# Performance work log

Measured on AMD Instinct MI355X. Metric: run time of the kernel, lower is better.

## Reference

```python
import jax, jax.numpy as jnp
import numpy as np

B, C, S = 256, 1024, 14   # batch, channels, spatial (frozen by y.view(b,c,14,14))
C2 = 15                   # channels2 in the module
CAT = C // 2 * 3 + C2     # 1551 = 15 + 512 + 1024
EPS = 1e-5


def _conv(x, w, b, groups, pad):
    out = jax.lax.conv_general_dilated(
        x, w, window_strides=(1, 1), padding=((pad, pad), (pad, pad)),
        dimension_numbers=('NCHW', 'OIHW', 'NCHW'), feature_group_count=groups)
    return out + b[None, :, None, None]


def _bn(x, gamma, beta):
    # training-mode BatchNorm2d: biased batch stats over (N,H,W)
    m = x.mean((0, 2, 3), keepdims=True)
    v = x.var((0, 2, 3), keepdims=True)
    return (x - m) * jax.lax.rsqrt(v + EPS) * gamma[None, :, None, None] + beta[None, :, None, None]


def setup_inputs() -> dict:
    key = jax.random.key(0)
    ks = jax.random.split(key, 16)
    r = C2 // 7  # = 2
    inp = {
        'y': jax.random.normal(ks[0], (B, C2, S * S), jnp.float32),
        'x': jax.random.normal(ks[1], (B, C, S, S), jnp.float32),
        'fc1_w': jax.random.normal(ks[2], (r, C2), jnp.float32) * 0.2,
        'fc2_w': jax.random.normal(ks[3], (C2, r), jnp.float32) * 0.2,
        'conv_w': jax.random.normal(ks[4], (C // 2, C, 1, 1), jnp.float32) * 0.03,
        'conv_b': jnp.zeros((C // 2,), jnp.float32),
        'dconv_w': jax.random.normal(ks[5], (C, 1, 3, 3), jnp.float32) * 0.2,
        'dconv_b': jnp.zeros((C,), jnp.float32),
        'dw1_w': jax.random.normal(ks[6], (CAT, 1, 3, 3), jnp.float32) * 0.2,
        'dw1_b': jnp.zeros((CAT,), jnp.float32),
        'pw1_w': jax.random.normal(ks[7], (C // 2, CAT, 1, 1), jnp.float32) * 0.03,
        'pw1_b': jnp.zeros((C // 2,), jnp.float32),
        'gamma': jnp.ones((C // 2,), jnp.float32),
        'beta': jnp.zeros((C // 2,), jnp.float32),
        'n': 0,
    }
    return inp


def reference(y, x, fc1_w, fc2_w, conv_w, conv_b, dconv_w, dconv_b,
              dw1_w, dw1_b, pw1_w, pw1_b, gamma, beta, n):
    b = y.shape[0]
    y4 = y.reshape(b, C2, S, S)
    # SE block on the 15 sub-channels
    g = y4.mean((2, 3))                              # (b, 15) global avg pool
    h = jax.nn.relu(g @ fc1_w.T) @ fc2_w.T           # (b, 15)
    y1 = y4 * jax.nn.sigmoid(h)[:, :, None, None]
    # depthwise conv on x, then per-(b,c) row covariance of the 14x14 map
    x1 = _conv(x, dconv_w, dconv_b, C, 1)            # (b, C, 14, 14)
    x2 = jax.lax.stop_gradient(x1)                   # .detach() in the original
    xc = x2 - x2.mean(-1, keepdims=True)             # np.cov: rows=vars, cols=obs
    cov = jnp.einsum('bcik,bcjk->bcij', xc, xc) / (S - 1)
    z = _conv(cov, conv_w, conv_b, 1, 0)             # 1x1 conv C -> C//2
    z = jax.nn.sigmoid(_bn(z, gamma, beta))
    for _ in range(n):                               # n=0 at these shapes
        y1 = jax.image.resize(y1, (y1.shape[0], y1.shape[1], y1.shape[2] * 2, y1.shape[3] * 2), 'bilinear')
    cat = jnp.concatenate([y1, z, x], axis=1)        # (b, 1551, 14, 14)
    o = _conv(cat, dw1_w, dw1_b, CAT, 1)             # depthwise 3x3
    o = _conv(o, pw1_w, pw1_b, 1, 0)                 # pointwise 1x1 -> C//2
    return jax.nn.relu(_bn(o, gamma, beta))
```

## Files before the change

kernel.cpp:

```cpp
#include <hip/hip_runtime.h>

typedef unsigned int u32;
typedef unsigned short u16;
typedef __attribute__((ext_vector_type(8))) short bf16x8;
typedef __attribute__((ext_vector_type(4))) float f32x4;
typedef __attribute__((ext_vector_type(4))) u32 u32x4;

#define EPSBN 1e-5f

#define GLDS16(gp, lp) __builtin_amdgcn_global_load_lds( \
    (const __attribute__((address_space(1))) u32*)(gp), \
    (__attribute__((address_space(3))) u32*)(lp), 16, 0, 0)

#define OFF_ADW    0ull
#define OFF_COVT   0ull
#define OFF_S      160563200ull
#define OFF_WBZ    160578560ull
#define OFF_WBP    161627136ull
#define OFF_STATSZ 163265536ull
#define OFF_STATSO 163269632ull
#define OFF_SCZ    163273728ull
#define OFF_SHZ    163275776ull
#define OFF_SCO    163277824ull
#define OFF_SHO    163279872ull

static __device__ __forceinline__ float bf2f(u16 h){
  u32 u = ((u32)h) << 16; float f; __builtin_memcpy(&f, &u, 4); return f;
}
static __device__ __forceinline__ u16 f2bf(float f){
  u32 u; __builtin_memcpy(&u, &f, 4);
  u = (u + 0x7fffu + ((u >> 16) & 1u)) >> 16;
  return (u16)u;
}

__global__ __launch_bounds__(64) void se_kernel(const float* __restrict__ y,
    const float* __restrict__ fc1, const float* __restrict__ fc2, float* __restrict__ sse){
  __shared__ float g[15];
  __shared__ float t[2];
  int b = blockIdx.x, l = threadIdx.x;
  for (int c = 0; c < 15; ++c){
    float p = 0.f;
    for (int k = l; k < 196; k += 64) p += y[((size_t)b*15 + c)*196 + k];
    p += __shfl_xor(p, 32); p += __shfl_xor(p, 16); p += __shfl_xor(p, 8);
    p += __shfl_xor(p, 4);  p += __shfl_xor(p, 2);  p += __shfl_xor(p, 1);
    if (l == 0) g[c] = p * (1.f/196.f);
  }
  __syncthreads();
  if (l < 2){
    float a = 0.f;
    for (int c = 0; c < 15; ++c) a += g[c] * fc1[l*15 + c];
    t[l] = fmaxf(a, 0.f);
  }
  __syncthreads();
  if (l < 15){
    float h = t[0]*fc2[l*2] + t[1]*fc2[l*2+1];
    sse[b*15 + l] = 1.f / (1.f + __expf(-h));
  }
}

__global__ void wconv_kernel(const float* __restrict__ cw, const float* __restrict__ pw,
                             u16* __restrict__ wbz, u16* __restrict__ wbp){
  u32 stride = gridDim.x * blockDim.x;
  for (u32 i = blockIdx.x*blockDim.x + threadIdx.x; i < 524288u; i += stride)
    wbz[i] = f2bf(cw[i]);
  for (u32 i = blockIdx.x*blockDim.x + threadIdx.x; i < 819200u; i += stride){
    u32 n = i / 1600u, k = i - n*1600u;
    wbp[i] = f2bf(k < 1551u ? pw[(size_t)n*1551 + k] : 0.f);
  }
}

__global__ __launch_bounds__(256,5) void cov_kernel(const float* __restrict__ x,
    const float* __restrict__ dcw, const float* __restrict__ dcb, u16* __restrict__ covT){
  __shared__ __align__(16) float xs[16*200];
  __shared__ __align__(16) u32 xcb[16*132];
  __shared__ float wls[16][9];
  __shared__ float wlb[16];
  u32* covL32 = (u32*)xs;

  int tid = threadIdx.x;
  int c0 = blockIdx.x * 16, b = blockIdx.y;

  {
    const float4* xg = (const float4*)(x + ((size_t)b*1024 + c0)*196);
    for (int i = tid; i < 784; i += 256){
      float4 v = xg[i];
      u32 c = (u32)i / 49u, p4 = (u32)i - c*49u;
      *(float4*)&xs[c*200u + p4*4u] = v;
    }
  }
  if (tid < 144) wls[tid/9][tid%9] = dcw[(size_t)(c0 + tid/9)*9 + (tid%9)];
  if (tid < 16) wlb[tid] = dcb[c0 + tid];
  __syncthreads();

  {
    int c = tid >> 4, i = tid & 15;
    u32 q[8];
    #pragma unroll
    for (int j = 0; j < 8; ++j) q[j] = 0u;
    if (i < 14){
      float wr[9];
      #pragma unroll
      for (int qq = 0; qq < 9; ++qq) wr[qq] = wls[c][qq];
      float topm = (i > 0) ? 1.f : 0.f, botm = (i < 13) ? 1.f : 0.f;
      wr[0] *= topm; wr[1] *= topm; wr[2] *= topm;
      wr[6] *= botm; wr[7] *= botm; wr[8] *= botm;
      float bb = wlb[c];
      float rr[3][16];
      #pragma unroll
      for (int d = 0; d < 3; ++d){
        rr[d][0] = 0.f; rr[d][15] = 0.f;
        int rowr = i + d - 1;
        rowr = rowr < 0 ? 0 : (rowr > 13 ? 13 : rowr);
        const float* src = &xs[c*200 + rowr*14];
        #pragma unroll
        for (int j = 0; j < 7; ++j)
          *(float2*)&rr[d][1 + 2*j] = *(const float2*)&src[2*j];
      }
      float ov[14];
      #pragma unroll
      for (int k = 0; k < 14; ++k){
        float a = bb;
        #pragma unroll
        for (int dy = 0; dy < 3; ++dy)
          #pragma unroll
          for (int dx = 0; dx < 3; ++dx)
            a += wr[dy*3+dx] * rr[dy][k + dx];
        ov[k] = a;
      }
      float mean = 0.f;
      #pragma unroll
      for (int k = 0; k < 14; ++k) mean += ov[k];
      mean *= (1.f/14.f);
      #pragma unroll
      for (int j = 0; j < 7; ++j){
        u32 lo = f2bf(ov[2*j]   - mean);
        u32 hi = f2bf(ov[2*j+1] - mean);
        q[j] = lo | (hi << 16);
      }
    }
    u32x4 q0 = {q[0], q[1], q[2], q[3]};
    u32x4 q1 = {q[4], q[5], q[6], q[7]};
    *(u32x4*)&xcb[c*132 + i*8]     = q0;
    *(u32x4*)&xcb[c*132 + i*8 + 4] = q1;
  }
  __syncthreads();

  {
    int w = tid >> 6, l = tid & 63, lr = l & 15, lq = l >> 4;
    #pragma unroll
    for (int pp = 0; pp < 2; ++pp){
      int clo = w*4 + 2*pp;
      bf16x8 alo = {0,0,0,0,0,0,0,0}, ahi = {0,0,0,0,0,0,0,0};
      if (lq < 2){
        alo = *(const bf16x8*)&xcb[clo*132 + lr*8 + lq*4];
        ahi = *(const bf16x8*)&xcb[(clo+1)*132 + lr*8 + lq*4];
      }
      f32x4 dlo = {0.f,0.f,0.f,0.f}, dhi = {0.f,0.f,0.f,0.f};
      dlo = __builtin_amdgcn_mfma_f32_16x16x32_bf16(alo, alo, dlo, 0, 0, 0);
      dhi = __builtin_amdgcn_mfma_f32_16x16x32_bf16(ahi, ahi, dhi, 0, 0, 0);
      if (lr < 14){
        int cp = w*2 + pp;
        #pragma unroll
        for (int r = 0; r < 4; ++r){
          int rowi = lq*4 + r;
          if (rowi < 14){
            u32 vv = (u32)f2bf(dlo[r] * (1.f/13.f)) | ((u32)f2bf(dhi[r] * (1.f/13.f)) << 16);
            covL32[cp*210 + rowi*14 + lr] = vv;
          }
        }
      }
    }
  }
  __syncthreads();

  for (int i = tid; i < 1568; i += 256){
    int cp = i & 7, ij = i >> 3;
    u32 v = covL32[cp*210 + ij];
    *(u32*)(covT + ((size_t)(b*196 + ij)*1024 + c0 + 2*cp)) = v;
  }
}

__global__ __launch_bounds__(256,5) void adw_kernel(
    const float* __restrict__ y, const float* __restrict__ sse,
    const u16* __restrict__ zT, const float* __restrict__ scz, const float* __restrict__ shz,
    const float* __restrict__ x, const float* __restrict__ dw1w, const float* __restrict__ dw1b,
    u16* __restrict__ Adw){
  __shared__ __align__(16) float ms[32*202];
  __shared__ float wd[32][9];
  __shared__ float bd[32];
  int tid = threadIdx.x;
  int cc0 = blockIdx.x * 32, b = blockIdx.y;

  for (int i = tid; i < 288; i += 256){
    int c = i / 9, q = i - c*9;
    int cc = cc0 + c;
    wd[c][q] = (cc < 1551) ? dw1w[(size_t)cc*9 + q] : 0.f;
  }
  if (tid < 32) bd[tid] = (cc0 + tid < 1551) ? dw1b[cc0 + tid] : 0.f;

  if (cc0 < 15){
    int ny = 15;
    for (int i = tid; i < ny*196; i += 256){
      u32 c = (u32)i / 196u, p = (u32)i - c*196u;
      ms[c*202u + p] = y[((size_t)b*15 + c)*196 + p] * sse[b*15 + c];
    }
  }
  {
    int zs = cc0 > 15 ? cc0 : 15;
    int ze = cc0 + 32 < 527 ? cc0 + 32 : 527;
    if (zs < ze){
      int nz = ze - zs, lbase = zs - cc0, obase = zs - 15;
      const u16* zrow = zT + (size_t)obase*50176 + (size_t)b*196;
      for (int i = tid; i < nz*98; i += 256){
        u32 oo = (u32)i / 98u, pp = (u32)i - oo*98u;
        u32 v = *(const u32*)(zrow + (size_t)oo*50176 + pp*2u);
        int o = obase + (int)oo;
        float s = scz[o], h = shz[o];
        float v0 = bf2f((u16)(v & 0xffffu)) * s + h;
        float v1 = bf2f((u16)(v >> 16))     * s + h;
        v0 = 1.f / (1.f + __expf(-v0));
        v1 = 1.f / (1.f + __expf(-v1));
        float2 fv = {v0, v1};
        *(float2*)&ms[(u32)(lbase + (int)oo)*202u + pp*2u] = fv;
      }
    }
  }
  {
    int xs_ = cc0 > 527 ? cc0 : 527;
    int xe = cc0 + 32 < 1551 ? cc0 + 32 : 1551;
    if (xs_ < xe){
      int nx = xe - xs_, lbase = xs_ - cc0, cxs = xs_ - 527;
      const float4* xg = (const float4*)(x + ((size_t)b*1024 + cxs)*196);
      for (int i = tid; i < nx*49; i += 256){
        float4 v = xg[i];
        u32 c = (u32)i / 49u, p4 = (u32)i - c*49u;
        float* dst = &ms[(u32)(lbase + (int)c)*202u + p4*4u];
        float2 lo = {v.x, v.y}, hi = {v.z, v.w};
        *(float2*)dst = lo;
        *(float2*)(dst + 2) = hi;
      }
    }
  }
  {
    int ps = cc0 > 1551 ? cc0 : 1551;
    int pe = cc0 + 32;
    if (ps < pe){
      int np = pe - ps, lbase = ps - cc0;
      for (int i = tid; i < np*196; i += 256){
        u32 c = (u32)i / 196u, p = (u32)i - c*196u;
        ms[(u32)(lbase + (int)c)*202u + p] = 0.f;
      }
    }
  }
  __syncthreads();

  for (int t = tid; t < 448; t += 256){
    int cc = t & 31, i = t >> 5;
    float wr[9];
    #pragma unroll
    for (int qq = 0; qq < 9; ++qq) wr[qq] = wd[cc][qq];
    float topm = (i > 0) ? 1.f : 0.f, botm = (i < 13) ? 1.f : 0.f;
    wr[0] *= topm; wr[1] *= topm; wr[2] *= topm;
    wr[6] *= botm; wr[7] *= botm; wr[8] *= botm;
    float bb = bd[cc];
    float rr[3][16];
    #pragma unroll
    for (int d = 0; d < 3; ++d){
      rr[d][0] = 0.f; rr[d][15] = 0.f;
      int rowr = i + d - 1;
      rowr = rowr < 0 ? 0 : (rowr > 13 ? 13 : rowr);
      const float* src = &ms[cc*202 + rowr*14];
      #pragma unroll
      for (int j = 0; j < 7; ++j)
        *(float2*)&rr[d][1 + 2*j] = *(const float2*)&src[2*j];
    }
    size_t obase = ((size_t)b*196 + i*14) * 1600 + cc0 + cc;
    #pragma unroll
    for (int k = 0; k < 14; ++k){
      float a = bb;
      #pragma unroll
      for (int dy = 0; dy < 3; ++dy)
        #pragma unroll
        for (int dx = 0; dx < 3; ++dx)
          a += wr[dy*3+dx] * rr[dy][k + dx];
      Adw[obase + (size_t)k*1600] = f2bf(a);
    }
  }
}

template<int MODE>
__global__ __launch_bounds__(256,3) void gemm_kernel(
    const u16* __restrict__ A, const u16* __restrict__ Bw,
    const float* __restrict__ bias, void* __restrict__ outp,
    float* __restrict__ stats, int K){
  __shared__ __align__(16) char smem[33280];
  u16* As = (u16*)smem;
  u16* Bs = (u16*)(smem + 16384);

  int tid = threadIdx.x;
  int w = tid >> 6, l = tid & 63;
  int wm = w >> 1, wn = w & 1;
  int lr = l & 15, lq = l >> 4;
  u32 g = blockIdx.x;
  u32 lin = (g & 7u) * 196u + (g >> 3);
  int n0 = (int)(lin & 3u) * 128;
  int m0 = (int)(lin >> 2) * 128;

  f32x4 acc[4][4] = {};
  int kTiles = K >> 6;

  for (int kt = 0; kt < kTiles; ++kt){
    if (kt) __syncthreads();
    #pragma unroll
    for (int i = 0; i < 4; ++i){
      int s = tid + i*256;
      int row = s >> 3, c8 = s & 7, sc = c8 ^ (row & 7);
      GLDS16(A  + (size_t)(m0 + row)*K + kt*64 + sc*8, As + s*8);
      GLDS16(Bw + (size_t)(n0 + row)*K + kt*64 + sc*8, Bs + s*8);
    }
    __syncthreads();
    #pragma unroll
    for (int ks = 0; ks < 2; ++ks){
      bf16x8 af[4], bfv[4];
      #pragma unroll
      for (int mi = 0; mi < 4; ++mi){
        int row = wm*64 + mi*16 + lr;
        int q = (ks*4 + lq) ^ (row & 7);
        af[mi] = *(const bf16x8*)(As + row*64 + q*8);
      }
      #pragma unroll
      for (int ni = 0; ni < 4; ++ni){
        int row = wn*64 + ni*16 + lr;
        int q = (ks*4 + lq) ^ (row & 7);
        bfv[ni] = *(const bf16x8*)(Bs + row*64 + q*8);
      }
      #pragma unroll
      for (int mi = 0; mi < 4; ++mi)
        #pragma unroll
        for (int ni = 0; ni < 4; ++ni)
          acc[mi][ni] = __builtin_amdgcn_mfma_f32_16x16x32_bf16(af[mi], bfv[ni], acc[mi][ni], 0, 0, 0);
    }
  }

  #pragma unroll
  for (int ni = 0; ni < 4; ++ni){
    int col = n0 + wn*64 + ni*16 + lr;
    float bb = bias[col];
    float s1 = 0.f, s2 = 0.f;
    #pragma unroll
    for (int mi = 0; mi < 4; ++mi)
      #pragma unroll
      for (int r = 0; r < 4; ++r){
        float v = acc[mi][ni][r] + bb;
        acc[mi][ni][r] = v;
        s1 += v; s2 += v*v;
      }
    s1 += __shfl_xor(s1, 16); s1 += __shfl_xor(s1, 32);
    s2 += __shfl_xor(s2, 16); s2 += __shfl_xor(s2, 32);
    if (lq == 0){
      atomicAdd(&stats[col], s1);
      atomicAdd(&stats[512 + col], s2);
    }
  }

  __syncthreads();
  float* eb = (float*)smem;
  #pragma unroll
  for (int rnd = 0; rnd < 2; ++rnd){
    if (wm == rnd){
      float* e = eb + wn * (64*65);
      #pragma unroll
      for (int mi = 0; mi < 4; ++mi)
        #pragma unroll
        for (int ni = 0; ni < 4; ++ni)
          #pragma unroll
          for (int r = 0; r < 4; ++r)
            e[(mi*16 + lq*4 + r)*65 + ni*16 + lr] = acc[mi][ni][r];
      int m = m0 + wm*64 + l;
      if (MODE == 0){
        u16* ob = (u16*)outp + (size_t)(n0 + wn*64)*50176 + m;
        #pragma unroll 8
        for (int no = 0; no < 64; ++no)
          ob[(size_t)no*50176] = f2bf(e[l*65 + no]);
      } else {
        u32 bq = (u32)m / 196u;
        u32 ij = (u32)m - bq*196u;
        float* ob = (float*)outp + ((size_t)bq*512 + n0 + wn*64)*196 + ij;
        #pragma unroll 8
        for (int no = 0; no < 64; ++no)
          ob[(size_t)no*196] = e[l*65 + no];
      }
    }
    __syncthreads();
  }
}

__global__ void bnprep_kernel(const float* __restrict__ stats, const float* __restrict__ gamma,
    const float* __restrict__ beta, float* __restrict__ sc, float* __restrict__ sh){
  int o = threadIdx.x;
  float m = stats[o] * (1.f/50176.f);
  float v = stats[512+o] * (1.f/50176.f) - m*m;
  float inv = rsqrtf(v + EPSBN);
  float g = gamma[o] * inv;
  sc[o] = g;
  sh[o] = beta[o] - m*g;
}

__global__ void final_kernel(float4* __restrict__ o4, const float* __restrict__ sc,
                             const float* __restrict__ sh){
  u32 stride = gridDim.x * blockDim.x;
  for (u32 i = blockIdx.x*blockDim.x + threadIdx.x; i < 6422528u; i += stride){
    u32 oc = (i / 49u) & 511u;
    float s = sc[oc], t = sh[oc];
    float4 v = o4[i];
    v.x = fmaxf(fmaf(v.x, s, t), 0.f);
    v.y = fmaxf(fmaf(v.y, s, t), 0.f);
    v.z = fmaxf(fmaf(v.z, s, t), 0.f);
    v.w = fmaxf(fmaf(v.w, s, t), 0.f);
    o4[i] = v;
  }
}

extern "C" void kernel_launch(void* const* d_in, const int* in_sizes, int n_in,
                              void* d_out, int out_size, void* d_ws, size_t ws_size,
                              hipStream_t stream){
  (void)in_sizes; (void)n_in; (void)out_size; (void)ws_size;
  const float* y      = (const float*)d_in[0];
  const float* x      = (const float*)d_in[1];
  const float* fc1    = (const float*)d_in[2];
  const float* fc2    = (const float*)d_in[3];
  const float* convw  = (const float*)d_in[4];
  const float* convb  = (const float*)d_in[5];
  const float* dconvw = (const float*)d_in[6];
  const float* dconvb = (const float*)d_in[7];
  const float* dw1w   = (const float*)d_in[8];
  const float* dw1b   = (const float*)d_in[9];
  const float* pw1w   = (const float*)d_in[10];
  const float* pw1b   = (const float*)d_in[11];
  const float* gamma  = (const float*)d_in[12];
  const float* beta   = (const float*)d_in[13];

  char* ws = (char*)d_ws;
  u16* covT   = (u16*)(ws + OFF_COVT);
  u16* Adw    = (u16*)(ws + OFF_ADW);
  float* sse  = (float*)(ws + OFF_S);
  u16* wbz    = (u16*)(ws + OFF_WBZ);
  u16* wbp    = (u16*)(ws + OFF_WBP);
  float* statsZ = (float*)(ws + OFF_STATSZ);
  float* statsO = (float*)(ws + OFF_STATSO);
  float* scz  = (float*)(ws + OFF_SCZ);
  float* shz  = (float*)(ws + OFF_SHZ);
  float* sco  = (float*)(ws + OFF_SCO);
  float* sho  = (float*)(ws + OFF_SHO);
  u16* zT     = (u16*)d_out;
  float* outf = (float*)d_out;

  hipMemsetAsync(statsZ, 0, 8192, stream);
  se_kernel<<<256, 64, 0, stream>>>(y, fc1, fc2, sse);
  wconv_kernel<<<2048, 256, 0, stream>>>(convw, pw1w, wbz, wbp);
  cov_kernel<<<dim3(64, 256), 256, 0, stream>>>(x, dconvw, dconvb, covT);
  gemm_kernel<0><<<1568, 256, 0, stream>>>(covT, wbz, convb, (void*)zT, statsZ, 1024);
  bnprep_kernel<<<1, 512, 0, stream>>>(statsZ, gamma, beta, scz, shz);
  adw_kernel<<<dim3(50, 256), 256, 0, stream>>>(y, sse, zT, scz, shz, x, dw1w, dw1b, Adw);
  gemm_kernel<1><<<1568, 256, 0, stream>>>(Adw, wbp, pw1b, (void*)outf, statsO, 1600);
  bnprep_kernel<<<1, 512, 0, stream>>>(statsO, gamma, beta, sco, sho);
  final_kernel<<<8192, 256, 0, stream>>>((float4*)outf, sco, sho);
}
```

Before: 516.6 us.

## Double-buffer GEMM LDS tiles to overlap global loads with MFMA compute

The GEMM K-loop now keeps two LDS buffers and prefetches the next 64-wide K tile with global_load_lds while MFMAs run on the current tile. This removes the load-then-compute serialization and one barrier per iteration. In exchange, LDS per block doubles to 64 KB and launch bounds drop from 3 to 2 blocks per CU, which lowers occupancy. The epilogue now reuses the same LDS array and relies on the loop's trailing barrier.

Result: no change. 526.8 us (+2.0%).

```diff
diff --git a/kernel.cpp b/kernel.cpp
--- a/kernel.cpp
+++ b/kernel.cpp
@@ -289,13 +289,11 @@
 }
 
 template<int MODE>
-__global__ __launch_bounds__(256,3) void gemm_kernel(
+__global__ __launch_bounds__(256,2) void gemm_kernel(
     const u16* __restrict__ A, const u16* __restrict__ Bw,
     const float* __restrict__ bias, void* __restrict__ outp,
     float* __restrict__ stats, int K){
-  __shared__ __align__(16) char smem[33280];
-  u16* As = (u16*)smem;
-  u16* Bs = (u16*)(smem + 16384);
+  __shared__ __align__(16) u16 lds[32768];
 
   int tid = threadIdx.x;
   int w = tid >> 6, l = tid & 63;
@@ -309,16 +307,32 @@
   f32x4 acc[4][4] = {};
   int kTiles = K >> 6;
 
+  const u16* Abase = A  + (size_t)m0*K;
+  const u16* Bbase = Bw + (size_t)n0*K;
+
+  #pragma unroll
+  for (int i = 0; i < 4; ++i){
+    int s = tid + i*256;
+    int row = s >> 3, c8 = s & 7, sc = c8 ^ (row & 7);
+    GLDS16(Abase + (size_t)row*K + sc*8, lds + s*8);
+    GLDS16(Bbase + (size_t)row*K + sc*8, lds + 8192 + s*8);
+  }
+  __syncthreads();
+
   for (int kt = 0; kt < kTiles; ++kt){
-    if (kt) __syncthreads();
-    #pragma unroll
-    for (int i = 0; i < 4; ++i){
-      int s = tid + i*256;
-      int row = s >> 3, c8 = s & 7, sc = c8 ^ (row & 7);
-      GLDS16(A  + (size_t)(m0 + row)*K + kt*64 + sc*8, As + s*8);
-      GLDS16(Bw + (size_t)(n0 + row)*K + kt*64 + sc*8, Bs + s*8);
-    }
-    __syncthreads();
+    u32 bufo = (u32)(kt & 1) * 16384u;
+    if (kt + 1 < kTiles){
+      u32 nbufo = bufo ^ 16384u;
+      #pragma unroll
+      for (int i = 0; i < 4; ++i){
+        int s = tid + i*256;
+        int row = s >> 3, c8 = s & 7, sc = c8 ^ (row & 7);
+        GLDS16(Abase + (size_t)row*K + (kt+1)*64 + sc*8, lds + nbufo + s*8);
+        GLDS16(Bbase + (size_t)row*K + (kt+1)*64 + sc*8, lds + nbufo + 8192 + s*8);
+      }
+    }
+    const u16* Ac = lds + bufo;
+    const u16* Bc = lds + bufo + 8192;
     #pragma unroll
     for (int ks = 0; ks < 2; ++ks){
       bf16x8 af[4], bfv[4];
@@ -326,13 +340,13 @@
       for (int mi = 0; mi < 4; ++mi){
         int row = wm*64 + mi*16 + lr;
         int q = (ks*4 + lq) ^ (row & 7);
-        af[mi] = *(const bf16x8*)(As + row*64 + q*8);
+        af[mi] = *(const bf16x8*)(Ac + row*64 + q*8);
       }
       #pragma unroll
       for (int ni = 0; ni < 4; ++ni){
         int row = wn*64 + ni*16 + lr;
         int q = (ks*4 + lq) ^ (row & 7);
-        bfv[ni] = *(const bf16x8*)(Bs + row*64 + q*8);
+        bfv[ni] = *(const bf16x8*)(Bc + row*64 + q*8);
       }
       #pragma unroll
       for (int mi = 0; mi < 4; ++mi)
@@ -340,6 +354,7 @@
         for (int ni = 0; ni < 4; ++ni)
           acc[mi][ni] = __builtin_amdgcn_mfma_f32_16x16x32_bf16(af[mi], bfv[ni], acc[mi][ni], 0, 0, 0);
     }
+    __syncthreads();
   }
 
   #pragma unroll
@@ -363,8 +378,7 @@
     }
   }
 
-  __syncthreads();
-  float* eb = (float*)smem;
+  float* eb = (float*)lds;
   #pragma unroll
   for (int rnd = 0; rnd < 2; ++rnd){
     if (wm == rnd){
```
